# Kernel tuning notes

Measured on AMD Instinct MI355X. Metric: run time of the kernel, lower is better.

The kernel has to match this reference:

```python
import jax, jax.numpy as jnp
import numpy as np

SR = 2            # search_range
LEAK = 0.2        # keras.activations.leaky_relu default negative_slope


def _conv(x, k, b):
    y = jax.lax.conv_general_dilated(x, k, (1, 1), 'SAME',
                                     dimension_numbers=('NHWC', 'HWIO', 'NHWC'))
    return y + b


def _lrelu(x):
    return jnp.where(x >= 0, x, LEAK * x)


def _bilinear_sample(imgs, cx, cy):
    # Faithful to the keras BilinearSampler: indices are PIXEL-flat (b*H*W + y*W + x)
    # but keras.ops.take flattens imgs over ALL dims (incl. channels), so the gather
    # reads from imgs.reshape(-1) at those pixel-flat positions and output has 1 channel.
    B, H, W, C = imgs.shape
    x0 = jnp.floor(cx); x1 = x0 + 1.0
    y0 = jnp.floor(cy); y1 = y0 + 1.0
    wt_x0 = x1 - cx; wt_x1 = cx - x0
    wt_y0 = y1 - cy; wt_y1 = cy - y0
    x_max = float(W - 1); y_max = float(H - 1)
    x0s = jnp.clip(x0, 0.0, x_max); x1s = jnp.clip(x1, 0.0, x_max)
    y0s = jnp.clip(y0, 0.0, y_max); y1s = jnp.clip(y1, 0.0, y_max)
    dim2 = float(W)
    base = (jnp.arange(B, dtype=jnp.float32) * float(H * W)).reshape(B, 1, 1, 1)
    by0 = base + y0s * dim2
    by1 = base + y1s * dim2
    flat = imgs.reshape(-1)
    g = lambda idx: jnp.take(flat, idx.astype(jnp.int32))
    im00 = g(x0s + by0); im01 = g(x0s + by1)
    im10 = g(x1s + by0); im11 = g(x1s + by1)
    return (wt_x0 * wt_y0) * im00 + (wt_x0 * wt_y1) * im01 \
         + (wt_x1 * wt_y0) * im10 + (wt_x1 * wt_y1) * im11


def _module_m(left, right, prev_disp, params):
    B, H, W, C = left.shape
    # upsample previous disparity to this level's resolution (bilinear, half-pixel)
    up = jax.image.resize(prev_disp, (B, H, W, 1), method='bilinear')
    # build sampling coords: x = j - flow, y = i (flow y-component is zeros)
    jj = jnp.arange(W, dtype=jnp.float32).reshape(1, 1, W, 1)
    ii = jnp.arange(H, dtype=jnp.float32).reshape(1, H, 1, 1)
    cx = jj - up                                   # [B,H,W,1]
    cy = jnp.broadcast_to(ii, (B, H, W, 1))        # [B,H,W,1]
    warped = _bilinear_sample(right, cx, cy)       # [B,H,W,1]
    # cost volume: shifted products, channel-mean (warped broadcasts over C)
    padded = jnp.pad(warped, ((0, 0), (0, 0), (SR, SR), (0, 0)))
    costs = [jnp.mean(left * padded[:, :, i:W + i, :], axis=3, keepdims=True)
             for i in range(2 * SR + 1)]
    cost_curve = jnp.concatenate([left] + costs, axis=-1)   # [B,H,W,C+5]
    vol = jnp.concatenate([cost_curve, up], axis=-1)        # [B,H,W,C+6]
    x = _lrelu(_conv(vol, params['k1'], params['b1']))
    x = _lrelu(_conv(x, params['k2'], params['b2']))
    x = _lrelu(_conv(x, params['k3'], params['b3']))
    x = _lrelu(_conv(x, params['k4'], params['b4']))
    x = _lrelu(_conv(x, params['k5'], params['b5']))
    x = _conv(x, params['k6'], params['b6'])                # linear head -> [B,H,W,1]
    return x


def setup_inputs() -> dict:
    key = jax.random.key(0)
    ks = jax.random.split(key, 16)
    B, H, W, C = 8, 128, 256, 128
    left = jax.random.normal(ks[0], (B, H, W, C), dtype=jnp.float32)
    right = jax.random.normal(ks[1], (B, H, W, C), dtype=jnp.float32)
    prev_disp = jax.random.uniform(ks[2], (B, H // 2, W // 2, 1), dtype=jnp.float32) * 8.0
    in_ch = C + (2 * SR + 1) + 1  # 134
    chans = [(in_ch, 128), (128, 128), (128, 96), (96, 64), (64, 32), (32, 1)]
    inp = {'left': left, 'right': right, 'prev_disp': prev_disp}
    for i, (ci, co) in enumerate(chans, start=1):
        inp[f'k{i}'] = jax.random.normal(ks[2 + 2 * i], (3, 3, ci, co), dtype=jnp.float32) * 0.05
        inp[f'b{i}'] = jnp.zeros((co,), dtype=jnp.float32)
    return inp


def reference(left, right, prev_disp, k1, b1, k2, b2, k3, b3, k4, b4, k5, b5, k6, b6):
    params = {'k1': k1, 'b1': b1, 'k2': k2, 'b2': b2, 'k3': k3, 'b3': b3,
              'k4': k4, 'b4': b4, 'k5': k5, 'b5': b5, 'k6': k6, 'b6': b6}
    return _module_m(left, right, prev_disp, params)
```

## Files before the change

### kernel.cpp

```cpp
#include <hip/hip_runtime.h>

typedef __attribute__((ext_vector_type(8))) short short8;
typedef __attribute__((ext_vector_type(4))) float f32x4;
typedef __attribute__((ext_vector_type(4))) unsigned short us4;

#define LEAK 0.2f

__device__ __forceinline__ float b2f(unsigned short s) {
    unsigned u = ((unsigned)s) << 16;
    return __builtin_bit_cast(float, u);
}
__device__ __forceinline__ unsigned short f2b(float f) {
    unsigned u = __builtin_bit_cast(unsigned, f);
    u += 0x7fffu + ((u >> 16) & 1u);
    return (unsigned short)(u >> 16);
}

__device__ __forceinline__ void async16(const short* g, short* l) {
    __builtin_amdgcn_global_load_lds(
        (const __attribute__((address_space(1))) void*)g,
        (__attribute__((address_space(3))) void*)l, 16, 0, 0);
}

__global__ __launch_bounds__(256)
void prep_kernel(const float* __restrict__ left, const float* __restrict__ right,
                 const float* __restrict__ pd, short* __restrict__ vol) {
    __shared__ __align__(16) float inL[64 * 132];
    __shared__ __align__(16) float rrow[256];
    __shared__ __align__(16) float pr0[128];
    __shared__ __align__(16) float pr1[128];
    __shared__ __align__(16) short outT[64 * 144];

    int t = threadIdx.x;
    int blk = blockIdx.x;
    int wq = blk & 3, h = (blk >> 2) & 127, b = blk >> 9;
    int w0 = wq << 6;

    float sy = h * 0.5f - 0.25f;
    float fy0 = floorf(sy);
    float fy = sy - fy0;
    int y0 = (int)fy0;
    int y0c = min(max(y0, 0), 63), y1c = min(max(y0 + 1, 0), 63);

    const float* lp = left + ((size_t)((b * 128 + h) * 256 + w0)) * 128;
#pragma unroll
    for (int k2 = 0; k2 < 8; ++k2) {
        int g = t + k2 * 256;
        int p = g >> 5, j = g & 31;
        float4 v = *(const float4*)(lp + (size_t)g * 4);
        *(float4*)(&inL[p * 132 + j * 4]) = v;
    }
    if (t < 64) {
        *(float4*)(&rrow[t * 4]) =
            *(const float4*)(right + ((size_t)(b * 128 + h)) * 256 + t * 4);
    } else if (t < 96) {
        int i2 = t - 64;
        *(float4*)(&pr0[i2 * 4]) = *(const float4*)(pd + (size_t)(b * 64 + y0c) * 128 + i2 * 4);
    } else if (t < 128) {
        int i2 = t - 96;
        *(float4*)(&pr1[i2 * 4]) = *(const float4*)(pd + (size_t)(b * 64 + y1c) * 128 + i2 * 4);
    }
    __syncthreads();

    int p = t >> 2, s = t & 3;
    int w = w0 + p;
    const float* src = &inL[p * 132 + s * 32];
    short* odst = &outT[p * 144 + s * 32];
    float sum = 0.f;
#pragma unroll
    for (int i = 0; i < 8; ++i) {
        float f0 = src[i * 4], f1 = src[i * 4 + 1], f2 = src[i * 4 + 2], f3 = src[i * 4 + 3];
        sum += (f0 + f1) + (f2 + f3);
        us4 o;
        o.x = f2b(f0); o.y = f2b(f1); o.z = f2b(f2); o.w = f2b(f3);
        *(us4*)(odst + i * 4) = o;
    }
    sum += __shfl_xor(sum, 1);
    sum += __shfl_xor(sum, 2);
    float mean = sum * (1.f / 128.f);

    float one_fy = 1.f - fy;
#pragma unroll
    for (int tap = s; tap < 5; tap += 4) {
        int jj = w + tap - 2;
        if (jj >= 0 && jj < 256) {
            float sx = jj * 0.5f - 0.25f;
            float fx0 = floorf(sx);
            float fx = sx - fx0;
            int x0 = (int)fx0;
            int x0c = min(max(x0, 0), 127), x1c = min(max(x0 + 1, 0), 127);
            float up = one_fy * ((1.f - fx) * pr0[x0c] + fx * pr0[x1c])
                     + fy     * ((1.f - fx) * pr1[x0c] + fx * pr1[x1c]);
            float cx = (float)jj - up;
            float xf0 = floorf(cx), xf1 = xf0 + 1.f;
            float w0x = xf1 - cx, w1x = cx - xf0;
            int ix0 = (int)fminf(fmaxf(xf0, 0.f), 255.f);
            int ix1 = (int)fminf(fmaxf(xf1, 0.f), 255.f);
            float warped = w0x * rrow[ix0] + w1x * rrow[ix1];
            outT[p * 144 + 128 + tap] = (short)f2b(warped * mean);
            if (tap == 2) outT[p * 144 + 133] = (short)f2b(up);
        } else {
            outT[p * 144 + 128 + tap] = 0;
        }
    }
    if (s == 0) { outT[p * 144 + 134] = 0; outT[p * 144 + 135] = 0; }
    if (s == 3) {
        us4 z = {};
        *(us4*)(&outT[p * 144 + 136]) = z;
        *(us4*)(&outT[p * 144 + 140]) = z;
    }
    __syncthreads();

    short* gdst = vol + ((size_t)(b * 130 + h + 1) * 258 + (w0 + 1)) * 144;
    for (int g = t; g < 1152; g += 256)
        *(short8*)(gdst + g * 8) = *(const short8*)(&outT[g * 8]);
}

__global__ void halo_zero_one(short* __restrict__ buf, int C) {
    int nchunk = C >> 3;
    int slot = blockIdx.x * 256 + threadIdx.x;
    int total = 8 * 772 * nchunk;
    if (slot >= total) return;
    int chunk = slot % nchunk;
    int pix = slot / nchunk;
    int b = pix / 772, p = pix % 772;
    int row, col;
    if (p < 516) { row = (p < 258) ? 0 : 129; col = (p < 258) ? p : p - 258; }
    else { int q = p - 516; row = 1 + (q >> 1); col = (q & 1) ? 257 : 0; }
    short8 z = {};
    *(short8*)(buf + ((size_t)(b * 130 + row) * 258 + col) * C + chunk * 8) = z;
}

__global__ void wconv_all(const float* __restrict__ k1, const float* __restrict__ k2,
                          const float* __restrict__ k3, const float* __restrict__ k4,
                          const float* __restrict__ k5,
                          short* __restrict__ w1, short* __restrict__ w2,
                          short* __restrict__ w3, short* __restrict__ w4,
                          short* __restrict__ w5) {
    const int CINt[5]  = {134, 128, 128, 96, 64};
    const int COUTt[5] = {128, 128, 96, 64, 32};
    const int KCt[5]   = {5, 4, 4, 3, 2};
    const float* srcs[5] = {k1, k2, k3, k4, k5};
    short* dsts[5] = {w1, w2, w3, w4, w5};
    int l = blockIdx.y;
    int CIN = CINt[l], COUT = COUTt[l], KC = KCt[l];
    const float* k = srcs[l];
    short* wt = dsts[l];
    int idx = blockIdx.x * 256 + threadIdx.x;
    int total = 9 * KC * COUT * 32;
    if (idx >= total) return;
    int kk = idx & 31;
    int rest = idx >> 5;
    int n = rest % COUT; rest /= COUT;
    int tap = rest % 9, kc = rest / 9;
    int ci = kc * 32 + kk;
    float v = (ci < CIN) ? k[(size_t)(tap * CIN + ci) * COUT + n] : 0.f;
    wt[idx] = (short)f2b(v);
}

template <int KC, int CIN_STR, int COUT, int NT, int LASTC>
__launch_bounds__(512, 2)
__global__ void conv3x3_kernel(const short* __restrict__ in, const short* __restrict__ wt,
                               const float* __restrict__ bias, short* __restrict__ out) {
    __shared__ short ldsA[6 * 130 * 4 * 8];
    __shared__ short ldsW[9 * COUT * 32];
    const int WSLOTS = 9 * COUT * 4;
    const int WSTRIDE = 9 * COUT * 32;

    int t = threadIdx.x;
    int lane = t & 63, wid = t >> 6;
    int q = lane >> 4, col = lane & 15;
    int out_row = wid >> 1, col_off = (wid & 1) << 6;

    int wtile = blockIdx.x & 1;
    int rest = blockIdx.x >> 1;
    int htile = rest & 31, b = rest >> 5;
    int w0h = wtile << 7;
    int row0 = htile << 2;

    const short* inbase = in + ((size_t)(b * 130 + row0) * 258 + w0h) * CIN_STR;

    f32x4 acc[4][NT] = {};

    for (int kc = 0; kc < KC; ++kc) {
        for (int i = t; i < 3120; i += 512) {
            int r = i / 520, rem = i % 520;
            int p = rem >> 2, s = rem & 3;
            int c = (s - p) & 3;
            if (LASTC == 4 || kc < KC - 1 || c < LASTC) {
                const short* g = inbase + ((size_t)r * 258 + p) * CIN_STR + kc * 32 + c * 8;
                async16(g, ldsA + (size_t)(i & ~63) * 8);
            }
        }
        {
            const short* wsrc = wt + (size_t)kc * WSTRIDE;
            for (int i = t; i < WSLOTS; i += 512)
                async16(wsrc + (size_t)i * 8, ldsW + (size_t)(i & ~63) * 8);
        }
        __syncthreads();

#pragma unroll
        for (int dy = 0; dy < 3; ++dy) {
#pragma unroll
            for (int dx = 0; dx < 3; ++dx) {
                int ldsrow = out_row + dy;
                short8 a[4], bfr[NT];
#pragma unroll
                for (int mt = 0; mt < 4; ++mt) {
                    int p = col_off + mt * 16 + col + dx;
                    a[mt] = *(const short8*)(ldsA +
                        (size_t)(((ldsrow * 130 + p) << 2) + ((q + p) & 3)) * 8);
                }
                const short* wp = ldsW + (size_t)(dy * 3 + dx) * COUT * 32;
#pragma unroll
                for (int nt = 0; nt < NT; ++nt)
                    bfr[nt] = *(const short8*)(wp + (nt * 16 + col) * 32 + q * 8);
#pragma unroll
                for (int mt = 0; mt < 4; ++mt)
#pragma unroll
                    for (int nt = 0; nt < NT; ++nt)
                        acc[mt][nt] = __builtin_amdgcn_mfma_f32_16x16x32_bf16(
                            a[mt], bfr[nt], acc[mt][nt], 0, 0, 0);
            }
        }
        __syncthreads();
    }

    size_t obase = ((size_t)(b * 130 + row0 + 1 + out_row) * 258 + (w0h + 1 + col_off)) * COUT;
#pragma unroll
    for (int nt = 0; nt < NT; ++nt) {
        int n = nt * 16 + col;
        float bv = bias[n];
#pragma unroll
        for (int mt = 0; mt < 4; ++mt) {
#pragma unroll
            for (int rr = 0; rr < 4; ++rr) {
                int m = mt * 16 + q * 4 + rr;
                float v = acc[mt][nt][rr] + bv;
                v = (v >= 0.f) ? v : LEAK * v;
                out[obase + (size_t)m * COUT + n] = (short)f2b(v);
            }
        }
    }
}

__global__ void conv6_kernel(const short* __restrict__ x, const float* __restrict__ k,
                             const float* __restrict__ bias, float* __restrict__ out) {
    __shared__ float wk[288];
    int t = threadIdx.x;
    for (int i = t; i < 288; i += 256) wk[i] = k[i];
    __syncthreads();
    int idx = blockIdx.x * 256 + t;
    int w = idx & 255, h = (idx >> 8) & 127, b = idx >> 15;
    float acc = bias[0];
#pragma unroll
    for (int dy = 0; dy < 3; ++dy) {
#pragma unroll
        for (int dx = 0; dx < 3; ++dx) {
            const short* xp = x + ((size_t)(b * 130 + h + dy) * 258 + (w + dx)) * 32;
            const float* wp = wk + (dy * 3 + dx) * 32;
#pragma unroll
            for (int c8 = 0; c8 < 4; ++c8) {
                short8 v = *(const short8*)(xp + c8 * 8);
#pragma unroll
                for (int j = 0; j < 8; ++j)
                    acc += b2f((unsigned short)v[j]) * wp[c8 * 8 + j];
            }
        }
    }
    out[idx] = acc;
}

extern "C" void kernel_launch(void* const* d_in, const int* in_sizes, int n_in,
                              void* d_out, int out_size, void* d_ws, size_t ws_size,
                              hipStream_t stream) {
    const float* left  = (const float*)d_in[0];
    const float* right = (const float*)d_in[1];
    const float* pd    = (const float*)d_in[2];
    const float* k[6];
    const float* bb[6];
    for (int i = 0; i < 6; ++i) { k[i] = (const float*)d_in[3 + 2 * i]; bb[i] = (const float*)d_in[4 + 2 * i]; }

    char* ws = (char*)d_ws;
    short* wt1 = (short*)ws;
    short* wt2 = (short*)(ws + 368640);
    short* wt3 = (short*)(ws + 663552);
    short* wt4 = (short*)(ws + 884736);
    short* wt5 = (short*)(ws + 995328);
    short* vol = (short*)(ws + 1048576);
    short* X1  = (short*)(ws + 1048576 + 77276160);
    short* X2  = vol;
    short* X3  = X1;
    short* X4  = vol;
    short* X5  = X1;

    auto hz = [&](short* buf, int C) {
        int blocks = (8 * 772 * (C >> 3) + 255) / 256;
        halo_zero_one<<<blocks, 256, 0, stream>>>(buf, C);
    };

    prep_kernel<<<4096, 256, 0, stream>>>(left, right, pd, vol);
    wconv_all<<<dim3(720, 5), 256, 0, stream>>>(k[0], k[1], k[2], k[3], k[4],
                                                wt1, wt2, wt3, wt4, wt5);
    hz(vol, 144);
    hz(X1, 128);

    conv3x3_kernel<5, 144, 128, 8, 2><<<512, 512, 0, stream>>>(vol, wt1, bb[0], X1);
    hz(X2, 128);
    conv3x3_kernel<4, 128, 128, 8, 4><<<512, 512, 0, stream>>>(X1, wt2, bb[1], X2);
    hz(X3, 96);
    conv3x3_kernel<4, 128,  96, 6, 4><<<512, 512, 0, stream>>>(X2, wt3, bb[2], X3);
    hz(X4, 64);
    conv3x3_kernel<3,  96,  64, 4, 4><<<512, 512, 0, stream>>>(X3, wt4, bb[3], X4);
    hz(X5, 32);
    conv3x3_kernel<2,  64,  32, 2, 4><<<512, 512, 0, stream>>>(X4, wt5, bb[4], X5);
    conv6_kernel<<<1024, 256, 0, stream>>>(X5, k[5], bb[5], (float*)d_out);
}
```

Before: 624.2 us.

## Double-buffer conv input tile in LDS and read weights from global

The conv kernel now keeps two LDS buffers for the input tile. It issues async loads for the next channel chunk after the first tap row, so the copy overlaps the MFMA work on the current chunk, and one barrier per iteration is removed. Weights are no longer staged through LDS; each lane reads its B fragments straight from global memory, relying on caches. The LDS swizzle changes from (q+p)&3 to (q+(p>>1))&3 to alter the bank-conflict pattern. The risk is global-load latency on the weight fragments inside the inner loop, plus higher LDS use from the two input buffers, which may affect two-blocks-per-CU occupancy.

```diff
diff --git a/kernel.cpp b/kernel.cpp
--- a/kernel.cpp
+++ b/kernel.cpp
@@ -162,10 +162,7 @@
 __launch_bounds__(512, 2)
 __global__ void conv3x3_kernel(const short* __restrict__ in, const short* __restrict__ wt,
                                const float* __restrict__ bias, short* __restrict__ out) {
-    __shared__ short ldsA[6 * 130 * 4 * 8];
-    __shared__ short ldsW[9 * COUT * 32];
-    const int WSLOTS = 9 * COUT * 4;
-    const int WSTRIDE = 9 * COUT * 32;
+    __shared__ short ldsA[2][6 * 130 * 4 * 8];
 
     int t = threadIdx.x;
     int lane = t & 63, wid = t >> 6;
@@ -180,38 +177,40 @@
 
     const short* inbase = in + ((size_t)(b * 130 + row0) * 258 + w0h) * CIN_STR;
 
-    f32x4 acc[4][NT] = {};
-
-    for (int kc = 0; kc < KC; ++kc) {
+    auto stage = [&](int skc, int d) {
+        short* dst = &ldsA[d][0];
         for (int i = t; i < 3120; i += 512) {
             int r = i / 520, rem = i % 520;
             int p = rem >> 2, s = rem & 3;
-            int c = (s - p) & 3;
-            if (LASTC == 4 || kc < KC - 1 || c < LASTC) {
-                const short* g = inbase + ((size_t)r * 258 + p) * CIN_STR + kc * 32 + c * 8;
-                async16(g, ldsA + (size_t)(i & ~63) * 8);
+            int c = (s - (p >> 1)) & 3;
+            if (LASTC == 4 || skc < KC - 1 || c < LASTC) {
+                const short* g = inbase + ((size_t)r * 258 + p) * CIN_STR + skc * 32 + c * 8;
+                async16(g, dst + (size_t)(i & ~63) * 8);
             }
         }
-        {
-            const short* wsrc = wt + (size_t)kc * WSTRIDE;
-            for (int i = t; i < WSLOTS; i += 512)
-                async16(wsrc + (size_t)i * 8, ldsW + (size_t)(i & ~63) * 8);
-        }
-        __syncthreads();
-
-#pragma unroll
-        for (int dy = 0; dy < 3; ++dy) {
+    };
+
+    f32x4 acc[4][NT] = {};
+
+    stage(0, 0);
+    __syncthreads();
+
+    for (int kc = 0; kc < KC; ++kc) {
+        const short* A = &ldsA[kc & 1][0];
+        const short* wk = wt + (size_t)kc * 9 * COUT * 32;
+
+        auto do_row = [&](int dy) {
+            int ldsrow = out_row + dy;
 #pragma unroll
             for (int dx = 0; dx < 3; ++dx) {
-                int ldsrow = out_row + dy;
                 short8 a[4], bfr[NT];
 #pragma unroll
                 for (int mt = 0; mt < 4; ++mt) {
                     int p = col_off + mt * 16 + col + dx;
-                    a[mt] = *(const short8*)(ldsA +
-                        (size_t)(((ldsrow * 130 + p) << 2) + ((q + p) & 3)) * 8);
+                    a[mt] = *(const short8*)(A +
+                        (size_t)(((ldsrow * 130 + p) << 2) + ((q + (p >> 1)) & 3)) * 8);
                 }
-                const short* wp = ldsW + (size_t)(dy * 3 + dx) * COUT * 32;
+                const short* wp = wk + (size_t)(dy * 3 + dx) * COUT * 32;
 #pragma unroll
                 for (int nt = 0; nt < NT; ++nt)
                     bfr[nt] = *(const short8*)(wp + (nt * 16 + col) * 32 + q * 8);
@@ -222,7 +221,12 @@
                         acc[mt][nt] = __builtin_amdgcn_mfma_f32_16x16x32_bf16(
                             a[mt], bfr[nt], acc[mt][nt], 0, 0, 0);
             }
-        }
+        };
+
+        do_row(0);
+        if (kc + 1 < KC) stage(kc + 1, (kc + 1) & 1);
+        do_row(1);
+        do_row(2);
         __syncthreads();
     }
 
```

New measurement: 766.3 us. 1.23x slower.

## Retile conv kernels to 64-wide tiles, split COUT across waves, double-buffer weights per row

Applied to the files above, without the earlier changes.

Shrinks each conv block's spatial tile from 128 to 64 columns and splits output channels across two wave halves, doubling the grid to 1024 blocks. Weights are staged one dy-row at a time into a double-buffered LDS area and prefetched while the current row computes. Weight layout is swizzled to avoid LDS bank conflicts, the block index is remapped for locality, and launch bounds now target 4 blocks per CU. The goal is higher occupancy and smaller LDS use, which pulls more latency hiding out of the CU. The cost is an extra barrier per dy row, less A-fragment reuse per wave, and higher register pressure.

```diff
diff --git a/kernel.cpp b/kernel.cpp
--- a/kernel.cpp
+++ b/kernel.cpp
@@ -149,72 +149,86 @@
     int idx = blockIdx.x * 256 + threadIdx.x;
     int total = 9 * KC * COUT * 32;
     if (idx >= total) return;
-    int kk = idx & 31;
+    int j = idx & 7;
+    int s = (idx >> 3) & 3;
     int rest = idx >> 5;
     int n = rest % COUT; rest /= COUT;
     int tap = rest % 9, kc = rest / 9;
+    int q = (s - n) & 3;
+    int kk = q * 8 + j;
     int ci = kc * 32 + kk;
     float v = (ci < CIN) ? k[(size_t)(tap * CIN + ci) * COUT + n] : 0.f;
     wt[idx] = (short)f2b(v);
 }
 
 template <int KC, int CIN_STR, int COUT, int NT, int LASTC>
-__launch_bounds__(512, 2)
+__launch_bounds__(512, 4)
 __global__ void conv3x3_kernel(const short* __restrict__ in, const short* __restrict__ wt,
                                const float* __restrict__ bias, short* __restrict__ out) {
-    __shared__ short ldsA[6 * 130 * 4 * 8];
-    __shared__ short ldsW[9 * COUT * 32];
-    const int WSLOTS = 9 * COUT * 4;
-    const int WSTRIDE = 9 * COUT * 32;
+    __shared__ short ldsA[6 * 66 * 4 * 8];
+    __shared__ short ldsW[2][3 * COUT * 32];
 
     int t = threadIdx.x;
     int lane = t & 63, wid = t >> 6;
     int q = lane >> 4, col = lane & 15;
-    int out_row = wid >> 1, col_off = (wid & 1) << 6;
-
-    int wtile = blockIdx.x & 1;
-    int rest = blockIdx.x >> 1;
+    int r = wid & 3, h = wid >> 2;
+    const int NH = COUT / 2;
+
+    int blk = blockIdx.x;
+    blk = (blk & 7) * 128 + (blk >> 3);
+    int wtile = blk & 3;
+    int rest = blk >> 2;
     int htile = rest & 31, b = rest >> 5;
-    int w0h = wtile << 7;
+    int w0h = wtile << 6;
     int row0 = htile << 2;
 
     const short* inbase = in + ((size_t)(b * 130 + row0) * 258 + w0h) * CIN_STR;
 
-    f32x4 acc[4][NT] = {};
-
-    for (int kc = 0; kc < KC; ++kc) {
-        for (int i = t; i < 3120; i += 512) {
-            int r = i / 520, rem = i % 520;
+    auto stageA = [&](int kc) {
+        for (int i = t; i < 1584; i += 512) {
+            int rr2 = i / 264, rem = i % 264;
             int p = rem >> 2, s = rem & 3;
             int c = (s - p) & 3;
             if (LASTC == 4 || kc < KC - 1 || c < LASTC) {
-                const short* g = inbase + ((size_t)r * 258 + p) * CIN_STR + kc * 32 + c * 8;
+                const short* g = inbase + ((size_t)rr2 * 258 + p) * CIN_STR + kc * 32 + c * 8;
                 async16(g, ldsA + (size_t)(i & ~63) * 8);
             }
         }
-        {
-            const short* wsrc = wt + (size_t)kc * WSTRIDE;
-            for (int i = t; i < WSLOTS; i += 512)
-                async16(wsrc + (size_t)i * 8, ldsW + (size_t)(i & ~63) * 8);
-        }
+    };
+    auto stageW = [&](int ph) {
+        const short* wsrc = wt + (size_t)(3 * ph) * COUT * 32;
+        short* dst = &ldsW[ph & 1][0];
+        for (int i = t; i < COUT * 12; i += 512)
+            async16(wsrc + (size_t)i * 8, dst + (size_t)(i & ~63) * 8);
+    };
+
+    f32x4 acc[4][NT] = {};
+
+    stageW(0);
+    for (int kc = 0; kc < KC; ++kc) {
+        stageA(kc);
         __syncthreads();
-
 #pragma unroll
         for (int dy = 0; dy < 3; ++dy) {
+            int ph = kc * 3 + dy;
+            if (ph + 1 < 3 * KC) stageW(ph + 1);
+            const short* WB = &ldsW[ph & 1][0];
+            int ldsrow = r + dy;
 #pragma unroll
             for (int dx = 0; dx < 3; ++dx) {
-                int ldsrow = out_row + dy;
                 short8 a[4], bfr[NT];
 #pragma unroll
                 for (int mt = 0; mt < 4; ++mt) {
-                    int p = col_off + mt * 16 + col + dx;
+                    int p = mt * 16 + col + dx;
                     a[mt] = *(const short8*)(ldsA +
-                        (size_t)(((ldsrow * 130 + p) << 2) + ((q + p) & 3)) * 8);
+                        (size_t)(((ldsrow * 66 + p) << 2) + ((q + p) & 3)) * 8);
                 }
-                const short* wp = ldsW + (size_t)(dy * 3 + dx) * COUT * 32;
-#pragma unroll
-                for (int nt = 0; nt < NT; ++nt)
-                    bfr[nt] = *(const short8*)(wp + (nt * 16 + col) * 32 + q * 8);
+#pragma unroll
+                for (int nt = 0; nt < NT; ++nt) {
+                    int n = h * NH + nt * 16 + col;
+                    bfr[nt] = *(const short8*)(WB +
+                        (size_t)((dx * COUT + n) * 4 + ((q + col) & 3)) * 8);
+                }
 #pragma unroll
                 for (int mt = 0; mt < 4; ++mt)
 #pragma unroll
@@ -222,15 +236,14 @@
                         acc[mt][nt] = __builtin_amdgcn_mfma_f32_16x16x32_bf16(
                             a[mt], bfr[nt], acc[mt][nt], 0, 0, 0);
             }
-        }
-        __syncthreads();
-    }
-
-    size_t obase = ((size_t)(b * 130 + row0 + 1 + out_row) * 258 + (w0h + 1 + col_off)) * COUT;
+            __syncthreads();
+        }
+    }
+
+    size_t obase = ((size_t)(b * 130 + row0 + 1 + r) * 258 + (w0h + 1)) * COUT + h * NH;
 #pragma unroll
     for (int nt = 0; nt < NT; ++nt) {
-        int n = nt * 16 + col;
-        float bv = bias[n];
+        float bv = bias[h * NH + nt * 16 + col];
 #pragma unroll
         for (int mt = 0; mt < 4; ++mt) {
 #pragma unroll
@@ -238,7 +251,7 @@
                 int m = mt * 16 + q * 4 + rr;
                 float v = acc[mt][nt][rr] + bv;
                 v = (v >= 0.f) ? v : LEAK * v;
-                out[obase + (size_t)m * COUT + n] = (short)f2b(v);
+                out[obase + (size_t)m * COUT + nt * 16 + col] = (short)f2b(v);
             }
         }
     }
@@ -305,14 +318,14 @@
     hz(vol, 144);
     hz(X1, 128);
 
-    conv3x3_kernel<5, 144, 128, 8, 2><<<512, 512, 0, stream>>>(vol, wt1, bb[0], X1);
+    conv3x3_kernel<5, 144, 128, 4, 2><<<1024, 512, 0, stream>>>(vol, wt1, bb[0], X1);
     hz(X2, 128);
-    conv3x3_kernel<4, 128, 128, 8, 4><<<512, 512, 0, stream>>>(X1, wt2, bb[1], X2);
+    conv3x3_kernel<4, 128, 128, 4, 4><<<1024, 512, 0, stream>>>(X1, wt2, bb[1], X2);
     hz(X3, 96);
-    conv3x3_kernel<4, 128,  96, 6, 4><<<512, 512, 0, stream>>>(X2, wt3, bb[2], X3);
+    conv3x3_kernel<4, 128,  96, 3, 4><<<1024, 512, 0, stream>>>(X2, wt3, bb[2], X3);
     hz(X4, 64);
-    conv3x3_kernel<3,  96,  64, 4, 4><<<512, 512, 0, stream>>>(X3, wt4, bb[3], X4);
+    conv3x3_kernel<3,  96,  64, 2, 4><<<1024, 512, 0, stream>>>(X3, wt4, bb[3], X4);
     hz(X5, 32);
-    conv3x3_kernel<2,  64,  32, 2, 4><<<512, 512, 0, stream>>>(X4, wt5, bb[4], X5);
+    conv3x3_kernel<2,  64,  32, 1, 4><<<1024, 512, 0, stream>>>(X4, wt5, bb[4], X5);
     conv6_kernel<<<1024, 256, 0, stream>>>(X5, k[5], bb[5], (float*)d_out);
 }
```

Measured after the change: 852.3 us. +36.5%, slower.
